# Kernel tuning notes

Hardware: AMD Instinct MI355X
Metric: run time of the kernel (lower is better)

The kernel has to match this reference:

```python
import jax, jax.numpy as jnp
import numpy as np

B, S, D, H = 4, 2048, 1024, 2048


def _two_linear_silu(x, w1, w2):
    # nn.Sequential(Linear(no bias), SiLU, Linear(no bias)); torch Linear: y = x @ W.T
    return jax.nn.silu(x @ w1.T) @ w2.T


def _l2norm(x, eps=1e-12):
    # F.normalize(p=2, dim=-1)
    return x / jnp.maximum(jnp.linalg.norm(x, axis=-1, keepdims=True), eps)


def _mem_mlp(x, w0, w1):
    # MemoryMLP with 2 layers: Linear(D->H,no bias), SiLU, Linear(H->D,no bias)
    return jax.nn.silu(x @ w0.T) @ w1.T


def setup_inputs() -> dict:
    key = jax.random.key(0)
    ks = jax.random.split(key, 16)
    p = lambda k, sh: (0.02 * jax.random.normal(k, sh)).astype(jnp.float32)
    return {
        "x": jax.random.normal(ks[0], (B, S, D), dtype=jnp.float32),
        "kp_w1": p(ks[1], (D, D)), "kp_w2": p(ks[2], (D, D)),
        "vp_w1": p(ks[3], (D, D)), "vp_w2": p(ks[4], (D, D)),
        "qp_w1": p(ks[5], (D, D)), "qp_w2": p(ks[6], (D, D)),
        "gd_w": p(ks[7], (D, D)), "gd_b": jnp.zeros((D,), jnp.float32),
        "gl_w": p(ks[8], (D, D)), "gl_b": jnp.zeros((D,), jnp.float32),
        "gm_w": p(ks[9], (D, D)), "gm_b": jnp.zeros((D,), jnp.float32),
        "mem_w0": p(ks[10], (H, D)), "mem_w1": p(ks[11], (D, H)),
        "mom0": jnp.zeros((H, D), jnp.float32),
        "mom1": jnp.zeros((D, H), jnp.float32),
        "out_w": p(ks[12], (D, D)),
    }


def reference(x, kp_w1, kp_w2, vp_w1, vp_w2, qp_w1, qp_w2,
              gd_w, gd_b, gl_w, gl_b, gm_w, gm_b,
              mem_w0, mem_w1, mom0, mom1, out_w):
    # K/V/Q projections (Linear-SiLU-Linear), then SiLU, then L2 normalize K/Q
    keys = jax.nn.silu(_two_linear_silu(x, kp_w1, kp_w2))
    values = jax.nn.silu(_two_linear_silu(x, vp_w1, vp_w2))
    queries = jax.nn.silu(_two_linear_silu(x, qp_w1, qp_w2))
    keys = _l2norm(keys)
    queries = _l2norm(queries)

    # Memory read with current state weights
    retrieved = _mem_mlp(queries, mem_w0, mem_w1)  # (B, S, D)

    # Data-dependent gates from mean-pooled input (scalar decay/lr/momentum)
    x_mean = x.mean(axis=1)  # (B, D)
    alpha = jax.nn.sigmoid(x_mean @ gd_w.T + gd_b).mean()  # decay
    theta = jax.nn.sigmoid(x_mean @ gl_w.T + gl_b).mean()  # learning rate
    eta = jax.nn.sigmoid(x_mean @ gm_w.T + gm_b).mean()    # momentum

    # Gradient of associative MSE loss w.r.t. memory weights (keys detached)
    def loss_fn(ws):
        w0, w1 = ws
        pred = _mem_mlp(jax.lax.stop_gradient(keys), w0, w1)
        return jnp.mean((pred - jax.lax.stop_gradient(values)) ** 2)

    g0, g1 = jax.grad(loss_fn)((mem_w0, mem_w1))

    # Surprise momentum + decayed weight update: S = eta*S - theta*grad ; W = (1-alpha)*W + S
    new_m0 = eta * mom0 - theta * g0
    new_m1 = eta * mom1 - theta * g1
    new_w0 = (1.0 - alpha) * mem_w0 + new_m0
    new_w1 = (1.0 - alpha) * mem_w1 + new_m1

    out = retrieved @ out_w.T  # proj_out (no bias)
    return out, new_w0, new_w1, new_m0, new_m1
```

## Files before the change

### kernel.cpp

```cpp
#include <hip/hip_runtime.h>
#include <hip/hip_bf16.h>
#include <stdint.h>

typedef unsigned short u16;
typedef u16 ushort8 __attribute__((ext_vector_type(8)));
typedef __bf16 bf16x8 __attribute__((ext_vector_type(8)));
typedef float f32x4 __attribute__((ext_vector_type(4)));

enum {
  EPI_F32S = 0,
  EPI_BF16 = 1,
  EPI_SILU = 2,
  EPI_SILU_PRE = 3,
  EPI_DIFF = 4,
  EPI_DSILU = 5,
  EPI_F32 = 6
};

__device__ __forceinline__ float bf2f(u16 u) {
  union { uint32_t i; float f; } c; c.i = ((uint32_t)u) << 16; return c.f;
}
__device__ __forceinline__ u16 f2bf(float f) {
  union { float f; uint32_t i; } c; c.f = f;
  uint32_t x = c.i;
  return (u16)((x + 0x7fffu + ((x >> 16) & 1u)) >> 16);
}
__device__ __forceinline__ float sigm(float x) { return 1.0f / (1.0f + __expf(-x)); }

__device__ __forceinline__ void async_ld16(const u16* g, const u16* l) {
  __builtin_amdgcn_global_load_lds(
      (const __attribute__((address_space(1))) void*)(uintptr_t)g,
      (__attribute__((address_space(3))) void*)(uint32_t)(uintptr_t)l,
      16, 0, 0);
}

__global__ __launch_bounds__(256)
void cvt_kernel(const float* __restrict__ in, u16* __restrict__ out, long n) {
  const long i = ((long)blockIdx.x * 256 + threadIdx.x) * 8;
  if (i >= n) return;
  f32x4 a = *(const f32x4*)(in + i);
  f32x4 b = *(const f32x4*)(in + i + 4);
  ushort8 v;
#pragma unroll
  for (int e = 0; e < 4; ++e) v[e] = f2bf(a[e]);
#pragma unroll
  for (int e = 0; e < 4; ++e) v[4 + e] = f2bf(b[e]);
  *(ushort8*)(out + i) = v;
}

template<int EPI>
__global__ __launch_bounds__(256)
void gemm_nt(const u16* __restrict__ A, const u16* __restrict__ B,
             void* Cp, const u16* X1, u16* X2,
             int M, int N, int K, int SK) {
  __shared__ u16 lA[4096];
  __shared__ u16 lB[4096];
  const int t = threadIdx.x;
  const int w = t >> 6, l = t & 63;
  const int nb = N >> 7;
  const int tilesPer = (M >> 7) * nb;
  int bid = blockIdx.x;
  const int ks = bid / tilesPer;
  bid -= ks * tilesPer;
  const int bm = bid / nb;
  const int bn = bid - bm * nb;
  const long mBase = (long)bm << 7;
  const long nBase = (long)bn << 7;
  const int wr = w >> 1, wc = w & 1;
  const int kLen = K / SK;

  f32x4 acc[4][4];
#pragma unroll
  for (int i = 0; i < 4; ++i)
#pragma unroll
    for (int j = 0; j < 4; ++j) acc[i][j] = f32x4{0.f, 0.f, 0.f, 0.f};

  const u16* gA = A + (mBase + (w << 4) + (l >> 2)) * (long)K + ((l & 3) << 3) + (long)ks * kLen;
  const u16* gB = B + (nBase + (w << 4) + (l >> 2)) * (long)K + ((l & 3) << 3) + (long)ks * kLen;
  const long rowStep = 64L * K;
  const u16* lAw = lA + (w << 9);
  const u16* lBw = lB + (w << 9);

  const int lr = l & 15;
  const int lk = (l >> 4) << 3;
  const int lg = l >> 4;

  for (int k0 = 0; k0 < kLen; k0 += 32) {
    __syncthreads();
    async_ld16(gA + k0, lAw);
    async_ld16(gA + k0 + rowStep, lAw + 2048);
    async_ld16(gB + k0, lBw);
    async_ld16(gB + k0 + rowStep, lBw + 2048);
    __syncthreads();
    bf16x8 av[4], bv[4];
#pragma unroll
    for (int m = 0; m < 4; ++m) {
      ushort8 u = *(const ushort8*)&lA[((wr << 6) + (m << 4) + lr) * 32 + lk];
      av[m] = __builtin_bit_cast(bf16x8, u);
    }
#pragma unroll
    for (int n = 0; n < 4; ++n) {
      ushort8 u = *(const ushort8*)&lB[((wc << 6) + (n << 4) + lr) * 32 + lk];
      bv[n] = __builtin_bit_cast(bf16x8, u);
    }
#pragma unroll
    for (int m = 0; m < 4; ++m)
#pragma unroll
      for (int n = 0; n < 4; ++n)
        acc[m][n] = __builtin_amdgcn_mfma_f32_16x16x32_bf16(av[m], bv[n], acc[m][n], 0, 0, 0);
  }

#pragma unroll
  for (int m = 0; m < 4; ++m) {
#pragma unroll
    for (int n = 0; n < 4; ++n) {
#pragma unroll
      for (int r = 0; r < 4; ++r) {
        const long row = mBase + (wr << 6) + (m << 4) + (lg << 2) + r;
        const long col = nBase + (wc << 6) + (n << 4) + lr;
        const long idx = row * N + col;
        const float v = acc[m][n][r];
        if constexpr (EPI == EPI_F32S) {
          ((float*)Cp)[(long)ks * M * N + idx] = v;
        } else if constexpr (EPI == EPI_F32) {
          ((float*)Cp)[idx] = v;
        } else if constexpr (EPI == EPI_BF16) {
          ((u16*)Cp)[idx] = f2bf(v);
        } else if constexpr (EPI == EPI_SILU) {
          ((u16*)Cp)[idx] = f2bf(v * sigm(v));
        } else if constexpr (EPI == EPI_SILU_PRE) {
          X2[idx] = f2bf(v);
          ((u16*)Cp)[idx] = f2bf(v * sigm(v));
        } else if constexpr (EPI == EPI_DIFF) {
          ((u16*)Cp)[idx] = f2bf(v - bf2f(X1[idx]));
        } else if constexpr (EPI == EPI_DSILU) {
          const float h = bf2f(X1[idx]);
          const float s = sigm(h);
          ((u16*)Cp)[idx] = f2bf(v * (s + h * s * (1.0f - s)));
        }
      }
    }
  }
}

__global__ __launch_bounds__(256)
void l2norm_kernel(u16* a) {
  const int w = threadIdx.x >> 6, l = threadIdx.x & 63;
  const long row = (long)blockIdx.x * 4 + w;
  u16* p = a + row * 1024 + l * 16;
  ushort8 v0 = *(const ushort8*)p;
  ushort8 v1 = *(const ushort8*)(p + 8);
  float ss = 0.0f;
#pragma unroll
  for (int e = 0; e < 8; ++e) { float f = bf2f(v0[e]); ss += f * f; }
#pragma unroll
  for (int e = 0; e < 8; ++e) { float f = bf2f(v1[e]); ss += f * f; }
#pragma unroll
  for (int off = 32; off >= 1; off >>= 1) ss += __shfl_xor(ss, off, 64);
  const float sc = 1.0f / fmaxf(sqrtf(ss), 1e-12f);
#pragma unroll
  for (int e = 0; e < 8; ++e) v0[e] = f2bf(bf2f(v0[e]) * sc);
#pragma unroll
  for (int e = 0; e < 8; ++e) v1[e] = f2bf(bf2f(v1[e]) * sc);
  *(ushort8*)p = v0;
  *(ushort8*)(p + 8) = v1;
}

__global__ __launch_bounds__(256)
void transpose_kernel(const u16* __restrict__ in, u16* __restrict__ out, int R, int C) {
  __shared__ u16 tile[64 * 72];
  const int t = threadIdx.x;
  const long br = blockIdx.y, bc = blockIdx.x;
#pragma unroll
  for (int i = 0; i < 2; ++i) {
    const int e = i * 256 + t;
    const int r = e >> 3, c0 = (e & 7) << 3;
    ushort8 v = *(const ushort8*)&in[(br * 64 + r) * C + bc * 64 + c0];
    *(ushort8*)&tile[r * 72 + c0] = v;
  }
  __syncthreads();
#pragma unroll
  for (int i = 0; i < 2; ++i) {
    const int e = i * 256 + t;
    const int r = e >> 3, c0 = (e & 7) << 3;
    ushort8 v;
#pragma unroll
    for (int j = 0; j < 8; ++j) v[j] = tile[(c0 + j) * 72 + r];
    *(ushort8*)&out[(bc * 64 + r) * R + br * 64 + c0] = v;
  }
}

__global__ __launch_bounds__(256)
void xmean_kernel(const float* __restrict__ x, float* __restrict__ xsum) {
  const int i = blockIdx.x * 256 + threadIdx.x;
  const int b = i >> 10, d = i & 1023;
  const int s0 = blockIdx.y << 7;
  const float* p = x + ((long)b * 2048 + s0) * 1024 + d;
  float s = 0.0f;
  for (int k = 0; k < 128; ++k) s += p[(long)k * 1024];
  atomicAdd(&xsum[i], s);
}

__global__ __launch_bounds__(256)
void gates_kernel(const float* __restrict__ xsum,
                  const float* __restrict__ W0, const float* __restrict__ b0,
                  const float* __restrict__ W1, const float* __restrict__ b1,
                  const float* __restrict__ W2, const float* __restrict__ b2,
                  float* __restrict__ gtmp) {
  const int gw = blockIdx.x * 4 + (threadIdx.x >> 6);
  const int l = threadIdx.x & 63;
  const int g = gw >> 12;
  const int rem = gw & 4095;
  const int b = rem >> 10, j = rem & 1023;
  const float* W = (g == 0) ? W0 : ((g == 1) ? W1 : W2);
  const float* bias = (g == 0) ? b0 : ((g == 1) ? b1 : b2);
  const float* xr = xsum + (b << 10) + (l << 4);
  const float* wrow = W + ((long)j << 10) + (l << 4);
  float s = 0.0f;
#pragma unroll
  for (int q = 0; q < 4; ++q) {
    f32x4 wv = *(const f32x4*)(wrow + q * 4);
    f32x4 xv = *(const f32x4*)(xr + q * 4);
#pragma unroll
    for (int e = 0; e < 4; ++e) s += wv[e] * xv[e];
  }
#pragma unroll
  for (int off = 32; off >= 1; off >>= 1) s += __shfl_xor(s, off, 64);
  if (l == 0) {
    const float z = s * (1.0f / 2048.0f) + bias[j];
    gtmp[gw] = sigm(z);
  }
}

__global__ __launch_bounds__(256)
void gatesum_kernel(const float* __restrict__ gtmp, float* __restrict__ gacc) {
  __shared__ float red[4];
  const int g = blockIdx.x, t = threadIdx.x;
  const float* p = gtmp + g * 4096;
  float s = 0.0f;
#pragma unroll
  for (int k = 0; k < 16; ++k) s += p[t + k * 256];
#pragma unroll
  for (int off = 32; off >= 1; off >>= 1) s += __shfl_xor(s, off, 64);
  if ((t & 63) == 0) red[t >> 6] = s;
  __syncthreads();
  if (t == 0) gacc[g] = red[0] + red[1] + red[2] + red[3];
}

__global__ __launch_bounds__(256)
void update_kernel(const float* __restrict__ graw, const float* __restrict__ w,
                   const float* __restrict__ mom, float* __restrict__ outw,
                   float* __restrict__ outm, const float* __restrict__ gacc,
                   float gscale, int n) {
  const int i = blockIdx.x * 256 + threadIdx.x;
  if (i >= n) return;
  const float alpha = gacc[0] * (1.0f / 4096.0f);
  const float theta = gacc[1] * (1.0f / 4096.0f);
  const float eta   = gacc[2] * (1.0f / 4096.0f);
  const float g4 = graw[i] + graw[i + (long)n] + graw[i + 2L * n] + graw[i + 3L * n];
  const float m_ = eta * mom[i] - theta * gscale * g4;
  const float w_ = (1.0f - alpha) * w[i] + m_;
  outm[i] = m_;
  outw[i] = w_;
}

extern "C" void kernel_launch(void* const* d_in, const int* in_sizes, int n_in,
                              void* d_out, int out_size, void* d_ws, size_t ws_size,
                              hipStream_t stream) {
  (void)in_sizes; (void)n_in; (void)out_size; (void)ws_size;
  const float* X   = (const float*)d_in[0];
  const float* KP1 = (const float*)d_in[1];
  const float* KP2 = (const float*)d_in[2];
  const float* VP1 = (const float*)d_in[3];
  const float* VP2 = (const float*)d_in[4];
  const float* QP1 = (const float*)d_in[5];
  const float* QP2 = (const float*)d_in[6];
  const float* GDW = (const float*)d_in[7];
  const float* GDB = (const float*)d_in[8];
  const float* GLW = (const float*)d_in[9];
  const float* GLB = (const float*)d_in[10];
  const float* GMW = (const float*)d_in[11];
  const float* GMB = (const float*)d_in[12];
  const float* W0  = (const float*)d_in[13];
  const float* W1  = (const float*)d_in[14];
  const float* M0  = (const float*)d_in[15];
  const float* M1  = (const float*)d_in[16];
  const float* OW  = (const float*)d_in[17];

  char* ws = (char*)d_ws;
  const size_t MB = (size_t)1 << 20;
  u16* X16  = (u16*)(ws + 0 * MB);
  u16* T1   = (u16*)(ws + 16 * MB);
  u16* KEYS = (u16*)(ws + 32 * MB);
  u16* VALS = (u16*)(ws + 48 * MB);
  u16* QUER = (u16*)(ws + 64 * MB);
  u16* AQ   = (u16*)(ws + 80 * MB);
  u16* HK   = (u16*)(ws + 112 * MB);
  u16* AKT  = (u16*)(ws + 144 * MB);
  u16* W1T  = (u16*)(ws + 176 * MB);
  u16* KP1b = (u16*)(ws + 180 * MB);
  u16* KP2b = (u16*)(ws + 182 * MB);
  u16* VP1b = (u16*)(ws + 184 * MB);
  u16* VP2b = (u16*)(ws + 186 * MB);
  u16* QP1b = (u16*)(ws + 188 * MB);
  u16* QP2b = (u16*)(ws + 190 * MB);
  u16* OWb  = (u16*)(ws + 192 * MB);
  u16* W0b  = (u16*)(ws + 194 * MB);
  u16* W1b  = (u16*)(ws + 198 * MB);
  float* G1R = (float*)(ws + 112 * MB);
  float* G0R = (float*)(ws + 0 * MB);
  float* XSUM = (float*)(ws + 202 * MB);
  float* GACC = (float*)(ws + 202 * MB + 16384);
  float* GTMP = (float*)(ws + 202 * MB + 20480);

  float* OUT0  = (float*)d_out;
  float* OUTW0 = OUT0 + 8388608;
  float* OUTW1 = OUTW0 + 2097152;
  float* OUTM0 = OUTW1 + 2097152;
  float* OUTM1 = OUTM0 + 2097152;

  hipMemsetAsync(XSUM, 0, 16384, stream);

  const dim3 blk(256);
#define GGRID(M_, N_, SK_) dim3((unsigned)(((M_) >> 7) * ((N_) >> 7) * (SK_)))

  cvt_kernel<<<4096, blk, 0, stream>>>(X, X16, 8388608);
  cvt_kernel<<<512, blk, 0, stream>>>(KP1, KP1b, 1048576);
  cvt_kernel<<<512, blk, 0, stream>>>(KP2, KP2b, 1048576);
  cvt_kernel<<<512, blk, 0, stream>>>(VP1, VP1b, 1048576);
  cvt_kernel<<<512, blk, 0, stream>>>(VP2, VP2b, 1048576);
  cvt_kernel<<<512, blk, 0, stream>>>(QP1, QP1b, 1048576);
  cvt_kernel<<<512, blk, 0, stream>>>(QP2, QP2b, 1048576);
  cvt_kernel<<<512, blk, 0, stream>>>(OW, OWb, 1048576);
  cvt_kernel<<<1024, blk, 0, stream>>>(W0, W0b, 2097152);
  cvt_kernel<<<1024, blk, 0, stream>>>(W1, W1b, 2097152);

  gemm_nt<EPI_SILU><<<GGRID(8192,1024,1), blk, 0, stream>>>(X16, KP1b, T1,   nullptr, nullptr, 8192, 1024, 1024, 1);
  gemm_nt<EPI_SILU><<<GGRID(8192,1024,1), blk, 0, stream>>>(T1,  KP2b, KEYS, nullptr, nullptr, 8192, 1024, 1024, 1);
  gemm_nt<EPI_SILU><<<GGRID(8192,1024,1), blk, 0, stream>>>(X16, VP1b, T1,   nullptr, nullptr, 8192, 1024, 1024, 1);
  gemm_nt<EPI_SILU><<<GGRID(8192,1024,1), blk, 0, stream>>>(T1,  VP2b, VALS, nullptr, nullptr, 8192, 1024, 1024, 1);
  gemm_nt<EPI_SILU><<<GGRID(8192,1024,1), blk, 0, stream>>>(X16, QP1b, T1,   nullptr, nullptr, 8192, 1024, 1024, 1);
  gemm_nt<EPI_SILU><<<GGRID(8192,1024,1), blk, 0, stream>>>(T1,  QP2b, QUER, nullptr, nullptr, 8192, 1024, 1024, 1);
  l2norm_kernel<<<2048, blk, 0, stream>>>(KEYS);
  l2norm_kernel<<<2048, blk, 0, stream>>>(QUER);

  gemm_nt<EPI_SILU><<<GGRID(8192,2048,1), blk, 0, stream>>>(QUER, W0b, AQ,   nullptr, nullptr, 8192, 2048, 1024, 1);
  gemm_nt<EPI_BF16><<<GGRID(8192,1024,1), blk, 0, stream>>>(AQ,   W1b, T1,   nullptr, nullptr, 8192, 1024, 2048, 1);
  gemm_nt<EPI_F32><<<GGRID(8192,1024,1), blk, 0, stream>>>(T1,   OWb, OUT0, nullptr, nullptr, 8192, 1024, 1024, 1);

  gemm_nt<EPI_SILU_PRE><<<GGRID(8192,2048,1), blk, 0, stream>>>(KEYS, W0b, AQ, nullptr, HK, 8192, 2048, 1024, 1);
  gemm_nt<EPI_DIFF><<<GGRID(8192,1024,1), blk, 0, stream>>>(AQ, W1b, T1, VALS, nullptr, 8192, 1024, 2048, 1);

  transpose_kernel<<<dim3(32,16), blk, 0, stream>>>(W1b, W1T, 1024, 2048);
  gemm_nt<EPI_DSILU><<<GGRID(8192,2048,1), blk, 0, stream>>>(T1, W1T, HK, HK, nullptr, 8192, 2048, 1024, 1);

  transpose_kernel<<<dim3(16,128), blk, 0, stream>>>(T1, VALS, 8192, 1024);
  transpose_kernel<<<dim3(32,128), blk, 0, stream>>>(AQ, AKT, 8192, 2048);
  transpose_kernel<<<dim3(32,128), blk, 0, stream>>>(HK, AQ, 8192, 2048);
  transpose_kernel<<<dim3(16,128), blk, 0, stream>>>(KEYS, QUER, 8192, 1024);

  gemm_nt<EPI_F32S><<<GGRID(1024,2048,4), blk, 0, stream>>>(VALS, AKT, G1R, nullptr, nullptr, 1024, 2048, 8192, 4);
  gemm_nt<EPI_F32S><<<GGRID(2048,1024,4), blk, 0, stream>>>(AQ, QUER, G0R, nullptr, nullptr, 2048, 1024, 8192, 4);

  xmean_kernel<<<dim3(16,16), blk, 0, stream>>>(X, XSUM);
  gates_kernel<<<3072, blk, 0, stream>>>(XSUM, GDW, GDB, GLW, GLB, GMW, GMB, GTMP);
  gatesum_kernel<<<3, blk, 0, stream>>>(GTMP, GACC);

  const float gscale = 2.0f / 8388608.0f;
  update_kernel<<<8192, blk, 0, stream>>>(G0R, W0, M0, OUTW0, OUTM0, GACC, gscale, 2097152);
  update_kernel<<<8192, blk, 0, stream>>>(G1R, W1, M1, OUTW1, OUTM1, GACC, gscale, 2097152);
#undef GGRID
}
```

Baseline: 984.1 us.

## Replace GEMM with 256x256 double-buffered swizzled kernel and fuse first-layer projections

Replaces the 128x128, 256-thread GEMM with a 256x256-tile, 512-thread kernel. It double-buffers K=64 slices in XOR-swizzled LDS and overlaps async loads with MFMA using vmcnt waits and priority hints. The three first-layer K/V/Q projections become one N=3072 GEMM over concatenated weights, with the second layers reading strided slices. Gradient GEMMs move to split-K 8 with a shared scratch buffer and 8-way reduction in the update kernel, and the workspace layout is reshuffled. The larger tiles cut global traffic but use 128 KB of LDS and many accumulator registers, which may limit occupancy, and the split-K GEMMs now have fewer output tiles.

```diff
diff --git a/kernel.cpp b/kernel.cpp
--- a/kernel.cpp
+++ b/kernel.cpp
@@ -49,74 +49,115 @@
 }
 
 template<int EPI>
-__global__ __launch_bounds__(256)
-void gemm_nt(const u16* __restrict__ A, const u16* __restrict__ B,
-             void* Cp, const u16* X1, u16* X2,
+__global__ __launch_bounds__(512, 2)
+void gemm256(const u16* __restrict__ A, int lda,
+             const u16* __restrict__ B, int ldb,
+             void* __restrict__ Cp, const u16* __restrict__ X1, u16* __restrict__ X2,
              int M, int N, int K, int SK) {
-  __shared__ u16 lA[4096];
-  __shared__ u16 lB[4096];
+  __shared__ u16 lds[65536];
   const int t = threadIdx.x;
   const int w = t >> 6, l = t & 63;
-  const int nb = N >> 7;
-  const int tilesPer = (M >> 7) * nb;
+  const int nb = N >> 8;
+  const int tilesPer = (M >> 8) * nb;
   int bid = blockIdx.x;
-  const int ks = bid / tilesPer;
-  bid -= ks * tilesPer;
-  const int bm = bid / nb;
-  const int bn = bid - bm * nb;
-  const long mBase = (long)bm << 7;
-  const long nBase = (long)bn << 7;
-  const int wr = w >> 1, wc = w & 1;
+  const int ks = bid / tilesPer; bid -= ks * tilesPer;
+  const int bm = bid / nb, bn = bid - bm * nb;
+  const long mBase = (long)bm << 8, nBase = (long)bn << 8;
   const int kLen = K / SK;
-
-  f32x4 acc[4][4];
-#pragma unroll
-  for (int i = 0; i < 4; ++i)
+  const int NT = kLen >> 6;
+  const int wr = w >> 2, wc = w & 3;
+  const int lr = l & 15, lh = l >> 4;
+
+  f32x4 acc[8][4];
+#pragma unroll
+  for (int i = 0; i < 8; ++i)
 #pragma unroll
     for (int j = 0; j < 4; ++j) acc[i][j] = f32x4{0.f, 0.f, 0.f, 0.f};
 
-  const u16* gA = A + (mBase + (w << 4) + (l >> 2)) * (long)K + ((l & 3) << 3) + (long)ks * kLen;
-  const u16* gB = B + (nBase + (w << 4) + (l >> 2)) * (long)K + ((l & 3) << 3) + (long)ks * kLen;
-  const long rowStep = 64L * K;
-  const u16* lAw = lA + (w << 9);
-  const u16* lBw = lB + (w << 9);
-
-  const int lr = l & 15;
-  const int lk = (l >> 4) << 3;
-  const int lg = l >> 4;
-
-  for (int k0 = 0; k0 < kLen; k0 += 32) {
-    __syncthreads();
-    async_ld16(gA + k0, lAw);
-    async_ld16(gA + k0 + rowStep, lAw + 2048);
-    async_ld16(gB + k0, lBw);
-    async_ld16(gB + k0 + rowStep, lBw + 2048);
-    __syncthreads();
-    bf16x8 av[4], bv[4];
-#pragma unroll
-    for (int m = 0; m < 4; ++m) {
-      ushort8 u = *(const ushort8*)&lA[((wr << 6) + (m << 4) + lr) * 32 + lk];
-      av[m] = __builtin_bit_cast(bf16x8, u);
+  const int colOff = (((l & 7) ^ (l >> 3)) << 3);
+  const long rowLoc = (w << 3) + (l >> 3);
+  const u16* gA = A + (mBase + rowLoc) * (long)lda + (long)ks * kLen + colOff;
+  const u16* gB = B + (nBase + rowLoc) * (long)ldb + (long)ks * kLen + colOff;
+
+  auto stage = [&](int buf, int kt) {
+    const long kOff = (long)kt << 6;
+    const u16* d = (const u16*)lds + buf * 32768 + (w << 9);
+#pragma unroll
+    for (int h = 0; h < 2; ++h)
+#pragma unroll
+      for (int r = 0; r < 2; ++r)
+        async_ld16(gA + ((h << 7) + (r << 6)) * (long)lda + kOff,
+                   d + (h << 13) + (r << 12));
+#pragma unroll
+    for (int h = 0; h < 2; ++h)
+#pragma unroll
+      for (int r = 0; r < 2; ++r)
+        async_ld16(gB + ((h << 7) + (r << 6)) * (long)ldb + kOff,
+                   d + 16384 + (h << 13) + (r << 12));
+  };
+
+  int cur = 0;
+  stage(0, 0);
+
+  const int swz = (lr & 7) << 3;
+  const int scol0 = ((lh << 3) + 0) ^ swz;
+  const int scol1 = ((lh << 3) + 32) ^ swz;
+  const int rowB0 = (wc & 1) << 6;
+
+  for (int kt = 0; kt < NT; ++kt) {
+    if (kt + 1 < NT) {
+      stage(cur ^ 1, kt + 1);
+      __builtin_amdgcn_sched_barrier(0);
+      asm volatile("s_waitcnt vmcnt(8)" ::: "memory");
+    } else {
+      asm volatile("s_waitcnt vmcnt(0)" ::: "memory");
     }
+    __builtin_amdgcn_s_barrier();
+    __builtin_amdgcn_sched_barrier(0);
+
+    const u16* cA = (const u16*)lds + cur * 32768 + wr * 8192;
+    const u16* cB = (const u16*)lds + cur * 32768 + 16384 + (wc >> 1) * 8192;
+
+#pragma unroll
+    for (int ksl = 0; ksl < 2; ++ksl) {
+      const int sc = ksl ? scol1 : scol0;
+      bf16x8 bfr[4];
+#pragma unroll
+      for (int n = 0; n < 4; ++n) {
+        const int row = rowB0 + (n << 4) + lr;
+        bfr[n] = __builtin_bit_cast(bf16x8, *(const ushort8*)(cB + row * 64 + sc));
+      }
+#pragma unroll
+      for (int g = 0; g < 2; ++g) {
+        bf16x8 afr[4];
+#pragma unroll
+        for (int mm = 0; mm < 4; ++mm) {
+          const int row = (((g << 2) + mm) << 4) + lr;
+          afr[mm] = __builtin_bit_cast(bf16x8, *(const ushort8*)(cA + row * 64 + sc));
+        }
+        __builtin_amdgcn_s_setprio(1);
+#pragma unroll
+        for (int mm = 0; mm < 4; ++mm)
+#pragma unroll
+          for (int n = 0; n < 4; ++n)
+            acc[(g << 2) + mm][n] =
+                __builtin_amdgcn_mfma_f32_16x16x32_bf16(afr[mm], bfr[n],
+                                                        acc[(g << 2) + mm][n], 0, 0, 0);
+        __builtin_amdgcn_s_setprio(0);
+        __builtin_amdgcn_s_barrier();
+        __builtin_amdgcn_sched_barrier(0);
+      }
+    }
+    cur ^= 1;
+  }
+
+#pragma unroll
+  for (int m = 0; m < 8; ++m) {
 #pragma unroll
     for (int n = 0; n < 4; ++n) {
-      ushort8 u = *(const ushort8*)&lB[((wc << 6) + (n << 4) + lr) * 32 + lk];
-      bv[n] = __builtin_bit_cast(bf16x8, u);
-    }
-#pragma unroll
-    for (int m = 0; m < 4; ++m)
-#pragma unroll
-      for (int n = 0; n < 4; ++n)
-        acc[m][n] = __builtin_amdgcn_mfma_f32_16x16x32_bf16(av[m], bv[n], acc[m][n], 0, 0, 0);
-  }
-
-#pragma unroll
-  for (int m = 0; m < 4; ++m) {
-#pragma unroll
-    for (int n = 0; n < 4; ++n) {
 #pragma unroll
       for (int r = 0; r < 4; ++r) {
-        const long row = mBase + (wr << 6) + (m << 4) + (lg << 2) + r;
+        const long row = mBase + (wr << 7) + (m << 4) + (lh << 2) + r;
         const long col = nBase + (wc << 6) + (n << 4) + lr;
         const long idx = row * N + col;
         const float v = acc[m][n][r];
@@ -257,8 +298,10 @@
   const float alpha = gacc[0] * (1.0f / 4096.0f);
   const float theta = gacc[1] * (1.0f / 4096.0f);
   const float eta   = gacc[2] * (1.0f / 4096.0f);
-  const float g4 = graw[i] + graw[i + (long)n] + graw[i + 2L * n] + graw[i + 3L * n];
-  const float m_ = eta * mom[i] - theta * gscale * g4;
+  float g8 = 0.0f;
+#pragma unroll
+  for (int s = 0; s < 8; ++s) g8 += graw[i + (long)s * n];
+  const float m_ = eta * mom[i] - theta * gscale * g8;
   const float w_ = (1.0f - alpha) * w[i] + m_;
   outm[i] = m_;
   outw[i] = w_;
@@ -292,26 +335,24 @@
   u16* X16  = (u16*)(ws + 0 * MB);
   u16* T1   = (u16*)(ws + 16 * MB);
   u16* KEYS = (u16*)(ws + 32 * MB);
-  u16* VALS = (u16*)(ws + 48 * MB);
-  u16* QUER = (u16*)(ws + 64 * MB);
-  u16* AQ   = (u16*)(ws + 80 * MB);
-  u16* HK   = (u16*)(ws + 112 * MB);
+  u16* HK   = (u16*)(ws + 48 * MB);
+  u16* VALS = (u16*)(ws + 80 * MB);
+  u16* QUER = (u16*)(ws + 96 * MB);
+  u16* AQ   = (u16*)(ws + 112 * MB);
   u16* AKT  = (u16*)(ws + 144 * MB);
-  u16* W1T  = (u16*)(ws + 176 * MB);
-  u16* KP1b = (u16*)(ws + 180 * MB);
-  u16* KP2b = (u16*)(ws + 182 * MB);
-  u16* VP1b = (u16*)(ws + 184 * MB);
-  u16* VP2b = (u16*)(ws + 186 * MB);
-  u16* QP1b = (u16*)(ws + 188 * MB);
-  u16* QP2b = (u16*)(ws + 190 * MB);
-  u16* OWb  = (u16*)(ws + 192 * MB);
-  u16* W0b  = (u16*)(ws + 194 * MB);
-  u16* W1b  = (u16*)(ws + 198 * MB);
-  float* G1R = (float*)(ws + 112 * MB);
-  float* G0R = (float*)(ws + 0 * MB);
-  float* XSUM = (float*)(ws + 202 * MB);
-  float* GACC = (float*)(ws + 202 * MB + 16384);
-  float* GTMP = (float*)(ws + 202 * MB + 20480);
+  u16* TKV  = (u16*)(ws + 144 * MB);
+  u16* W1T  = (u16*)(ws + 192 * MB);
+  u16* WCAT = (u16*)(ws + 196 * MB);
+  u16* KP2b = (u16*)(ws + 202 * MB);
+  u16* VP2b = (u16*)(ws + 204 * MB);
+  u16* QP2b = (u16*)(ws + 206 * MB);
+  u16* OWb  = (u16*)(ws + 208 * MB);
+  u16* W0b  = (u16*)(ws + 210 * MB);
+  u16* W1b  = (u16*)(ws + 214 * MB);
+  float* GR   = (float*)(ws + 16 * MB);
+  float* XSUM = (float*)(ws + 218 * MB);
+  float* GACC = (float*)(ws + 218 * MB + 16384);
+  float* GTMP = (float*)(ws + 218 * MB + 20480);
 
   float* OUT0  = (float*)d_out;
   float* OUTW0 = OUT0 + 8388608;
@@ -321,53 +362,49 @@
 
   hipMemsetAsync(XSUM, 0, 16384, stream);
 
-  const dim3 blk(256);
-#define GGRID(M_, N_, SK_) dim3((unsigned)(((M_) >> 7) * ((N_) >> 7) * (SK_)))
+  const dim3 blk(256), blk512(512);
+#define G256(M_, N_, SK_) dim3((unsigned)(((M_) >> 8) * ((N_) >> 8) * (SK_)))
 
   cvt_kernel<<<4096, blk, 0, stream>>>(X, X16, 8388608);
-  cvt_kernel<<<512, blk, 0, stream>>>(KP1, KP1b, 1048576);
+  cvt_kernel<<<512, blk, 0, stream>>>(KP1, WCAT, 1048576);
+  cvt_kernel<<<512, blk, 0, stream>>>(VP1, WCAT + 1048576, 1048576);
+  cvt_kernel<<<512, blk, 0, stream>>>(QP1, WCAT + 2097152, 1048576);
   cvt_kernel<<<512, blk, 0, stream>>>(KP2, KP2b, 1048576);
-  cvt_kernel<<<512, blk, 0, stream>>>(VP1, VP1b, 1048576);
   cvt_kernel<<<512, blk, 0, stream>>>(VP2, VP2b, 1048576);
-  cvt_kernel<<<512, blk, 0, stream>>>(QP1, QP1b, 1048576);
   cvt_kernel<<<512, blk, 0, stream>>>(QP2, QP2b, 1048576);
   cvt_kernel<<<512, blk, 0, stream>>>(OW, OWb, 1048576);
   cvt_kernel<<<1024, blk, 0, stream>>>(W0, W0b, 2097152);
   cvt_kernel<<<1024, blk, 0, stream>>>(W1, W1b, 2097152);
-
-  gemm_nt<EPI_SILU><<<GGRID(8192,1024,1), blk, 0, stream>>>(X16, KP1b, T1,   nullptr, nullptr, 8192, 1024, 1024, 1);
-  gemm_nt<EPI_SILU><<<GGRID(8192,1024,1), blk, 0, stream>>>(T1,  KP2b, KEYS, nullptr, nullptr, 8192, 1024, 1024, 1);
-  gemm_nt<EPI_SILU><<<GGRID(8192,1024,1), blk, 0, stream>>>(X16, VP1b, T1,   nullptr, nullptr, 8192, 1024, 1024, 1);
-  gemm_nt<EPI_SILU><<<GGRID(8192,1024,1), blk, 0, stream>>>(T1,  VP2b, VALS, nullptr, nullptr, 8192, 1024, 1024, 1);
-  gemm_nt<EPI_SILU><<<GGRID(8192,1024,1), blk, 0, stream>>>(X16, QP1b, T1,   nullptr, nullptr, 8192, 1024, 1024, 1);
-  gemm_nt<EPI_SILU><<<GGRID(8192,1024,1), blk, 0, stream>>>(T1,  QP2b, QUER, nullptr, nullptr, 8192, 1024, 1024, 1);
+  transpose_kernel<<<dim3(32, 16), blk, 0, stream>>>(W1b, W1T, 1024, 2048);
+
+  xmean_kernel<<<dim3(16, 16), blk, 0, stream>>>(X, XSUM);
+  gates_kernel<<<3072, blk, 0, stream>>>(XSUM, GDW, GDB, GLW, GLB, GMW, GMB, GTMP);
+  gatesum_kernel<<<3, blk, 0, stream>>>(GTMP, GACC);
+
+  gemm256<EPI_SILU><<<G256(8192, 3072, 1), blk512, 0, stream>>>(X16, 1024, WCAT, 1024, TKV, nullptr, nullptr, 8192, 3072, 1024, 1);
+  gemm256<EPI_SILU><<<G256(8192, 1024, 1), blk512, 0, stream>>>(TKV + 0, 3072, KP2b, 1024, KEYS, nullptr, nullptr, 8192, 1024, 1024, 1);
+  gemm256<EPI_SILU><<<G256(8192, 1024, 1), blk512, 0, stream>>>(TKV + 1024, 3072, VP2b, 1024, VALS, nullptr, nullptr, 8192, 1024, 1024, 1);
+  gemm256<EPI_SILU><<<G256(8192, 1024, 1), blk512, 0, stream>>>(TKV + 2048, 3072, QP2b, 1024, QUER, nullptr, nullptr, 8192, 1024, 1024, 1);
   l2norm_kernel<<<2048, blk, 0, stream>>>(KEYS);
   l2norm_kernel<<<2048, blk, 0, stream>>>(QUER);
 
-  gemm_nt<EPI_SILU><<<GGRID(8192,2048,1), blk, 0, stream>>>(QUER, W0b, AQ,   nullptr, nullptr, 8192, 2048, 1024, 1);
-  gemm_nt<EPI_BF16><<<GGRID(8192,1024,1), blk, 0, stream>>>(AQ,   W1b, T1,   nullptr, nullptr, 8192, 1024, 2048, 1);
-  gemm_nt<EPI_F32><<<GGRID(8192,1024,1), blk, 0, stream>>>(T1,   OWb, OUT0, nullptr, nullptr, 8192, 1024, 1024, 1);
-
-  gemm_nt<EPI_SILU_PRE><<<GGRID(8192,2048,1), blk, 0, stream>>>(KEYS, W0b, AQ, nullptr, HK, 8192, 2048, 1024, 1);
-  gemm_nt<EPI_DIFF><<<GGRID(8192,1024,1), blk, 0, stream>>>(AQ, W1b, T1, VALS, nullptr, 8192, 1024, 2048, 1);
-
-  transpose_kernel<<<dim3(32,16), blk, 0, stream>>>(W1b, W1T, 1024, 2048);
-  gemm_nt<EPI_DSILU><<<GGRID(8192,2048,1), blk, 0, stream>>>(T1, W1T, HK, HK, nullptr, 8192, 2048, 1024, 1);
-
-  transpose_kernel<<<dim3(16,128), blk, 0, stream>>>(T1, VALS, 8192, 1024);
-  transpose_kernel<<<dim3(32,128), blk, 0, stream>>>(AQ, AKT, 8192, 2048);
-  transpose_kernel<<<dim3(32,128), blk, 0, stream>>>(HK, AQ, 8192, 2048);
-  transpose_kernel<<<dim3(16,128), blk, 0, stream>>>(KEYS, QUER, 8192, 1024);
-
-  gemm_nt<EPI_F32S><<<GGRID(1024,2048,4), blk, 0, stream>>>(VALS, AKT, G1R, nullptr, nullptr, 1024, 2048, 8192, 4);
-  gemm_nt<EPI_F32S><<<GGRID(2048,1024,4), blk, 0, stream>>>(AQ, QUER, G0R, nullptr, nullptr, 2048, 1024, 8192, 4);
-
-  xmean_kernel<<<dim3(16,16), blk, 0, stream>>>(X, XSUM);
-  gates_kernel<<<3072, blk, 0, stream>>>(XSUM, GDW, GDB, GLW, GLB, GMW, GMB, GTMP);
-  gatesum_kernel<<<3, blk, 0, stream>>>(GTMP, GACC);
+  gemm256<EPI_SILU><<<G256(8192, 2048, 1), blk512, 0, stream>>>(QUER, 1024, W0b, 1024, AQ, nullptr, nullptr, 8192, 2048, 1024, 1);
+  gemm256<EPI_BF16><<<G256(8192, 1024, 1), blk512, 0, stream>>>(AQ, 2048, W1b, 2048, T1, nullptr, nullptr, 8192, 1024, 2048, 1);
+  gemm256<EPI_F32><<<G256(8192, 1024, 1), blk512, 0, stream>>>(T1, 1024, OWb, 1024, OUT0, nullptr, nullptr, 8192, 1024, 1024, 1);
+
+  gemm256<EPI_SILU_PRE><<<G256(8192, 2048, 1), blk512, 0, stream>>>(KEYS, 1024, W0b, 1024, AQ, nullptr, HK, 8192, 2048, 1024, 1);
+  gemm256<EPI_DIFF><<<G256(8192, 1024, 1), blk512, 0, stream>>>(AQ, 2048, W1b, 2048, T1, VALS, nullptr, 8192, 1024, 2048, 1);
+  gemm256<EPI_DSILU><<<G256(8192, 2048, 1), blk512, 0, stream>>>(T1, 1024, W1T, 1024, HK, HK, nullptr, 8192, 2048, 1024, 1);
+
+  transpose_kernel<<<dim3(16, 128), blk, 0, stream>>>(T1, VALS, 8192, 1024);
+  transpose_kernel<<<dim3(32, 128), blk, 0, stream>>>(AQ, AKT, 8192, 2048);
+  transpose_kernel<<<dim3(32, 128), blk, 0, stream>>>(HK, AQ, 8192, 2048);
+  transpose_kernel<<<dim3(16, 128), blk, 0, stream>>>(KEYS, QUER, 8192, 1024);
 
   const float gscale = 2.0f / 8388608.0f;
-  update_kernel<<<8192, blk, 0, stream>>>(G0R, W0, M0, OUTW0, OUTM0, GACC, gscale, 2097152);
-  update_kernel<<<8192, blk, 0, stream>>>(G1R, W1, M1, OUTW1, OUTM1, GACC, gscale, 2097152);
-#undef GGRID
-}
+  gemm256<EPI_F32S><<<G256(1024, 2048, 8), blk512, 0, stream>>>(VALS, 8192, AKT, 8192, GR, nullptr, nullptr, 1024, 2048, 8192, 8);
+  update_kernel<<<8192, blk, 0, stream>>>(GR, W1, M1, OUTW1, OUTM1, GACC, gscale, 2097152);
+  gemm256<EPI_F32S><<<G256(2048, 1024, 8), blk512, 0, stream>>>(AQ, 8192, QUER, 8192, GR, nullptr, nullptr, 2048, 1024, 8192, 8);
+  update_kernel<<<8192, blk, 0, stream>>>(GR, W0, M0, OUTW0, OUTM0, GACC, gscale, 2097152);
+#undef G256
+}
```

New measurement: 894.0 us. 1.1x faster.
